# Optimization experiments

Hardware: AMD Instinct MI355X
Metric: run time of the kernel (lower is better)

The kernel has to match this reference:

```python
import jax, jax.numpy as jnp
import numpy as np

D = 128
N_DATA = 100000
N_TASK = 20000
E = 1000000


def _conv_params(key, d):
    ks = jax.random.split(key, 9)
    s = 1.0 / np.sqrt(d)
    return dict(
        Wmn=jax.random.uniform(ks[0], (d, d), jnp.float32, -s, s),
        bmn=jnp.zeros((d,), jnp.float32),
        Wme=jax.random.uniform(ks[1], (d, 1), jnp.float32, -1.0, 1.0),
        bme=jnp.zeros((d,), jnp.float32),
        Wgn=jax.random.uniform(ks[2], (d, d), jnp.float32, -s, s),
        bgn=jnp.zeros((d,), jnp.float32),
        Wge=jax.random.uniform(ks[3], (d, 1), jnp.float32, -1.0, 1.0),
        bge=jnp.zeros((d,), jnp.float32),
        bias=jnp.zeros((d,), jnp.float32),  # HeteConvLayer bias, zeros-init
    )


def setup_inputs() -> dict:
    key = jax.random.key(0)
    ks = jax.random.split(key, 12)
    inp = {
        'x_data': jax.random.normal(ks[0], (N_DATA, D), jnp.float32),
        'x_task': jax.random.normal(ks[1], (N_TASK, D), jnp.float32),
        'src_dt': jax.random.randint(ks[2], (E,), 0, N_DATA, jnp.int32),
        'dst_dt': jax.random.randint(ks[3], (E,), 0, N_TASK, jnp.int32),
        'ef_dt': jax.random.uniform(ks[4], (E, 1), jnp.float32),
        'src_td': jax.random.randint(ks[5], (E,), 0, N_TASK, jnp.int32),
        'dst_td': jax.random.randint(ks[6], (E,), 0, N_DATA, jnp.int32),
        'ef_td': jax.random.uniform(ks[7], (E, 1), jnp.float32),
    }
    # two separate HeteConvLayers (cfg.kg.hete=True)
    for name, k in (('dt', ks[8]), ('td', ks[9])):
        for pn, pv in _conv_params(k, D).items():
            inp[pn + '_' + name] = pv
    s = 1.0 / np.sqrt(D)
    inp['Ws_data'] = jax.random.uniform(ks[10], (D, D), jnp.float32, -s, s)
    inp['bs_data'] = jnp.zeros((D,), jnp.float32)
    inp['Ws_task'] = jax.random.uniform(ks[11], (D, D), jnp.float32, -s, s)
    inp['bs_task'] = jnp.zeros((D,), jnp.float32)
    return inp


def _hete_conv(x_neigh, src, dst, ef, Wmn, bmn, Wme, bme, Wgn, bgn, Wge, bge, bias, n_out):
    xj = x_neigh[src]                                   # [E, D] gather
    msg = xj @ Wmn.T + bmn + ef @ Wme.T + bme           # [E, D]
    gate = jax.nn.sigmoid(xj @ Wgn.T + bgn + ef @ Wge.T + bge) - 0.5  # gate_bias
    msg = msg * gate
    return jax.ops.segment_sum(msg, dst, num_segments=n_out) + bias


def _self_layer(x, Ws, bs):
    return (jax.nn.sigmoid(x @ Ws.T + bs) + 0.5) * x    # SelfLayer, gate_bias=True


def reference(x_data, x_task, src_dt, dst_dt, ef_dt, src_td, dst_td, ef_td,
              Wmn_dt, bmn_dt, Wme_dt, bme_dt, Wgn_dt, bgn_dt, Wge_dt, bge_dt, bias_dt,
              Wmn_td, bmn_td, Wme_td, bme_td, Wgn_td, bgn_td, Wge_td, bge_td, bias_td,
              Ws_data, bs_data, Ws_task, bs_task):
    # message type (data, property, task): neigh=data, self=task
    agg_task = _hete_conv(x_data, src_dt, dst_dt, ef_dt,
                          Wmn_dt, bmn_dt, Wme_dt, bme_dt,
                          Wgn_dt, bgn_dt, Wge_dt, bge_dt, bias_dt, N_TASK)
    # message type (task, property, data): neigh=task, self=data
    agg_data = _hete_conv(x_task, src_td, dst_td, ef_td,
                          Wmn_td, bmn_td, Wme_td, bme_td,
                          Wgn_td, bgn_td, Wge_td, bge_td, bias_td, N_DATA)
    # add self-transform, aggr='add', then Postlayer = ReLU
    data_emb = jax.nn.relu(agg_data + _self_layer(x_data, Ws_data, bs_data))
    task_emb = jax.nn.relu(agg_task + _self_layer(x_task, Ws_task, bs_task))
    # concatenate node-type outputs along node axis for a single output array
    return jnp.concatenate([data_emb, task_emb], axis=0)
```

## Files before the change

### kernel.cpp

```cpp
#include <hip/hip_runtime.h>
#include <hip/hip_bf16.h>
#include <cstdint>
#include <cstddef>

#define D_DIM 128

typedef __attribute__((ext_vector_type(8))) short short8;
typedef __attribute__((ext_vector_type(4))) float f32x4;

__device__ __forceinline__ float sigmoid_fast(float z) {
  return __builtin_amdgcn_rcpf(1.0f + __expf(-z));
}

__device__ __forceinline__ unsigned short f2bf(float f) {
  union { float f; unsigned u; } v; v.f = f;
  unsigned r = v.u + 0x7FFF + ((v.u >> 16) & 1);
  return (unsigned short)(r >> 16);
}
__device__ __forceinline__ float bf_lo(unsigned u) { return __uint_as_float(u << 16); }
__device__ __forceinline__ float bf_hi(unsigned u) { return __uint_as_float(u & 0xFFFF0000u); }

__global__ __launch_bounds__(256) void wconv_kernel(
    const float* __restrict__ s0, const float* __restrict__ s1, const float* __restrict__ s2,
    const float* __restrict__ s3, const float* __restrict__ s4, const float* __restrict__ s5,
    short* __restrict__ dst) {
  int idx = blockIdx.x * 256 + threadIdx.x;
  int mat = idx >> 12;
  int pos = (idx & 4095) * 4;
  const float* s = (mat == 0) ? s0 : (mat == 1) ? s1 : (mat == 2) ? s2
                 : (mat == 3) ? s3 : (mat == 4) ? s4 : s5;
  float4 f = *(const float4*)(s + pos);
  short4 o;
  o.x = (short)f2bf(f.x); o.y = (short)f2bf(f.y);
  o.z = (short)f2bf(f.z); o.w = (short)f2bf(f.w);
  *(short4*)(dst + mat * 16384 + pos) = o;
}

__global__ __launch_bounds__(256) void node_mfma_kernel(
    const float* __restrict__ x,
    const short* __restrict__ Wmnb, const short* __restrict__ Wgnb, const short* __restrict__ Wsb,
    const float* __restrict__ bmn, const float* __restrict__ bme,
    const float* __restrict__ bgn, const float* __restrict__ bge,
    const float* __restrict__ bs, const float* __restrict__ bias_other,
    unsigned int* __restrict__ YG, float* __restrict__ out_init, int n) {
  __shared__ unsigned sh[32][132];
  const int t = threadIdx.x;
  const int wave = t >> 6, lane = t & 63;
  const int q = lane >> 4, l15 = lane & 15;
  const int ng = wave >> 1;
  const int h = (wave & 1) * 64;
  const int base_node = blockIdx.x * 32;
  const int node_base = base_node + ng * 16;

  short8 a[4];
  {
    int m = node_base + l15;
    int mc = m < n ? m : (n - 1);
    const float* xrow = x + (size_t)mc * D_DIM;
#pragma unroll
    for (int ks = 0; ks < 4; ++ks) {
      float4 f0 = *(const float4*)(xrow + ks * 32 + q * 8);
      float4 f1 = *(const float4*)(xrow + ks * 32 + q * 8 + 4);
      union { short8 s; __hip_bfloat162 hh[4]; } u;
      u.hh[0] = __float22bfloat162_rn({f0.x, f0.y});
      u.hh[1] = __float22bfloat162_rn({f0.z, f0.w});
      u.hh[2] = __float22bfloat162_rn({f1.x, f1.y});
      u.hh[3] = __float22bfloat162_rn({f1.z, f1.w});
      a[ks] = u.s;
    }
  }

  f32x4 accY[4], accG[4], accS[4];
#pragma unroll
  for (int nt = 0; nt < 4; ++nt) { accY[nt] = {0,0,0,0}; accG[nt] = {0,0,0,0}; accS[nt] = {0,0,0,0}; }

#pragma unroll
  for (int nt = 0; nt < 4; ++nt) {
    const int row = h + nt * 16 + l15;
#pragma unroll
    for (int ks = 0; ks < 4; ++ks) {
      const int off = row * D_DIM + ks * 32 + q * 8;
      short8 bm  = *(const short8*)(Wmnb + off);
      short8 bg  = *(const short8*)(Wgnb + off);
      short8 bsw = *(const short8*)(Wsb + off);
      accY[nt] = __builtin_amdgcn_mfma_f32_16x16x32_bf16(a[ks], bm,  accY[nt], 0, 0, 0);
      accG[nt] = __builtin_amdgcn_mfma_f32_16x16x32_bf16(a[ks], bg,  accG[nt], 0, 0, 0);
      accS[nt] = __builtin_amdgcn_mfma_f32_16x16x32_bf16(a[ks], bsw, accS[nt], 0, 0, 0);
    }
  }

#pragma unroll
  for (int nt = 0; nt < 4; ++nt) {
    int d = h + nt * 16 + l15;
    float bmv = bmn[d] + bme[d];
    float bgv = bgn[d] + bge[d];
#pragma unroll
    for (int r = 0; r < 4; ++r) {
      union { __hip_bfloat162 hh; unsigned u; } pck;
      pck.hh = __float22bfloat162_rn({accY[nt][r] + bmv, accG[nt][r] + bgv});
      sh[ng * 16 + q * 4 + r][d] = pck.u;
    }
  }
  __syncthreads();
#pragma unroll
  for (int it = 0; it < 4; ++it) {
    int idx = (it * 256 + t) * 4;
    int nl = idx >> 7, dd = idx & 127;
    int node = base_node + nl;
    if (node < n)
      *(uint4*)(YG + (size_t)node * D_DIM + dd) = *(const uint4*)&sh[nl][dd];
  }
  __syncthreads();

  float* shf = (float*)sh;
#pragma unroll
  for (int nt = 0; nt < 4; ++nt) {
    int d = h + nt * 16 + l15;
    float bsv = bs[d];
#pragma unroll
    for (int r = 0; r < 4; ++r)
      shf[(ng * 16 + q * 4 + r) * 132 + d] = sigmoid_fast(accS[nt][r] + bsv) + 0.5f;
  }
  __syncthreads();
#pragma unroll
  for (int it = 0; it < 4; ++it) {
    int idx = (it * 256 + t) * 4;
    int nl = idx >> 7, dd = idx & 127;
    int node = base_node + nl;
    if (node < n) {
      float4 xv = *(const float4*)(x + (size_t)node * D_DIM + dd);
      float4 bo = *(const float4*)(bias_other + dd);
      const float* sp = &shf[nl * 132 + dd];
      float4 o;
      o.x = sp[0] * xv.x + bo.x;
      o.y = sp[1] * xv.y + bo.y;
      o.z = sp[2] * xv.z + bo.z;
      o.w = sp[3] * xv.w + bo.w;
      *(float4*)(out_init + (size_t)node * D_DIM + dd) = o;
    }
  }
}


__global__ __launch_bounds__(256) void hist0_kernel(
    const int* __restrict__ dst_dt, const int* __restrict__ dst_td,
    int* __restrict__ ghist, int nbt, int NB, int E) {
  __shared__ int lh[768];
  int t = threadIdx.x;
  lh[t] = 0; lh[t + 256] = 0; lh[t + 512] = 0;
  __syncthreads();
  for (int i = blockIdx.x * 256 + t; i < E; i += gridDim.x * 256) {
    atomicAdd(&lh[dst_dt[i] >> 6], 1);
    atomicAdd(&lh[nbt + (dst_td[i] >> 8)], 1);
  }
  __syncthreads();
#pragma unroll
  for (int k = 0; k < 3; ++k) {
    int b = t + k * 256;
    int c = lh[b];
    if (b < NB && c) atomicAdd(&ghist[b], c);
  }
}

__global__ __launch_bounds__(256) void bucket_scan_kernel(
    const int* __restrict__ ghist, int* __restrict__ bbase, int* __restrict__ bcur,
    int* __restrict__ offsets, int NB, int n_tot) {
  __shared__ int sc[256];
  int t = threadIdx.x;
  int i0 = t * 3;
  int c0 = (i0     < NB) ? ghist[i0]     : 0;
  int c1 = (i0 + 1 < NB) ? ghist[i0 + 1] : 0;
  int c2 = (i0 + 2 < NB) ? ghist[i0 + 2] : 0;
  int tot = c0 + c1 + c2;
  sc[t] = tot; __syncthreads();
  for (int s = 1; s < 256; s <<= 1) {
    int u = (t >= s) ? sc[t - s] : 0;
    __syncthreads(); sc[t] += u; __syncthreads();
  }
  int base = sc[t] - tot;
  if (i0     < NB) { bbase[i0]     = base;           bcur[i0]     = base; }
  if (i0 + 1 < NB) { bbase[i0 + 1] = base + c0;      bcur[i0 + 1] = base + c0; }
  if (i0 + 2 < NB) { bbase[i0 + 2] = base + c0 + c1; bcur[i0 + 2] = base + c0 + c1; }
  if (t == 255) { bbase[NB] = sc[255]; offsets[n_tot] = sc[255]; }
}

__global__ __launch_bounds__(256) void sort_a_kernel(
    const int* __restrict__ src_dt, const int* __restrict__ dst_dt, const float* __restrict__ ef_dt,
    const int* __restrict__ src_td, const int* __restrict__ dst_td, const float* __restrict__ ef_td,
    int* __restrict__ bcur, int2* __restrict__ eA, int nbt, int NB, int E) {
  __shared__ int lh[768];
  __shared__ int lcur[768];
  int t = threadIdx.x;
  lh[t] = 0; lh[t + 256] = 0; lh[t + 512] = 0;
  __syncthreads();
  int e0 = blockIdx.x * 4096;
  int e1 = min(E, e0 + 4096);
  for (int i = e0 + t; i < e1; i += 256) {
    atomicAdd(&lh[dst_dt[i] >> 6], 1);
    atomicAdd(&lh[nbt + (dst_td[i] >> 8)], 1);
  }
  __syncthreads();
#pragma unroll
  for (int k = 0; k < 3; ++k) {
    int b = t + k * 256;
    int c = lh[b];
    if (b < NB && c) lcur[b] = atomicAdd(&bcur[b], c);
  }
  __syncthreads();
  for (int i = e0 + t; i < e1; i += 256) {
    int c = dst_dt[i];
    int bkt = c >> 6;
    int pos = atomicAdd(&lcur[bkt], 1);
    eA[pos] = make_int2(src_dt[i],
        (int)((__float_as_uint(ef_dt[i]) & 0xFFFFFF00u) | (unsigned)(c & 63)));
    int cd = dst_td[i];
    int bkt2 = nbt + (cd >> 8);
    int pos2 = atomicAdd(&lcur[bkt2], 1);
    eA[pos2] = make_int2(src_td[i],
        (int)((__float_as_uint(ef_td[i]) & 0xFFFFFF00u) | (unsigned)(cd & 255)));
  }
}

__global__ __launch_bounds__(256) void sort_b_kernel(
    const int2* __restrict__ eA, const int* __restrict__ bbase,
    int* __restrict__ offsets, int2* __restrict__ eB,
    int nbt, int n_task, int n_tot) {
  __shared__ int lh[256], sc[256], lcur[256];
  int b = blockIdx.x, t = threadIdx.x;
  int base = bbase[b];
  int cnt = bbase[b + 1] - base;
  int c0, nloc;
  if (b < nbt) { c0 = b << 6; nloc = min(64, n_task - c0); }
  else { c0 = n_task + ((b - nbt) << 8); nloc = min(256, n_tot - c0); }
  lh[t] = 0; __syncthreads();
  for (int i = base + t; i < base + cnt; i += 256)
    atomicAdd(&lh[((unsigned)eA[i].y) & 255u], 1);
  __syncthreads();
  int v = lh[t];
  sc[t] = v; __syncthreads();
  for (int s = 1; s < 256; s <<= 1) {
    int u = (t >= s) ? sc[t - s] : 0;
    __syncthreads(); sc[t] += u; __syncthreads();
  }
  int ex = sc[t] - v;
  lcur[t] = base + ex;
  if (t < nloc) offsets[c0 + t] = base + ex;
  __syncthreads();
  for (int i = base + t; i < base + cnt; i += 256) {
    int2 e = eA[i];
    int pos = atomicAdd(&lcur[((unsigned)e.y) & 255u], 1);
    eB[pos] = e;
  }
}

__device__ __forceinline__ void gstep(float2& acc, int2 e, const unsigned* __restrict__ YG,
                                      int lane, float2 wme, float2 wge) {
  uint2 yg = *(const uint2*)(YG + (size_t)e.x * D_DIM + 2 * lane);
  float f = __int_as_float(e.y & (int)0xFFFFFF00);
  float g0 = sigmoid_fast(fmaf(f, wge.x, bf_hi(yg.x))) - 0.5f;
  float g1 = sigmoid_fast(fmaf(f, wge.y, bf_hi(yg.y))) - 0.5f;
  acc.x += fmaf(f, wme.x, bf_lo(yg.x)) * g0;
  acc.y += fmaf(f, wme.y, bf_lo(yg.y)) * g1;
}

__global__ __launch_bounds__(256) void gather_kernel(
    const unsigned* __restrict__ YG_dt, const unsigned* __restrict__ YG_td,
    const int* __restrict__ offsets, const int2* __restrict__ edata,
    const float* __restrict__ Wme_dt, const float* __restrict__ Wge_dt,
    const float* __restrict__ Wme_td, const float* __restrict__ Wge_td,
    float* __restrict__ out, int n_task, int n_data) {
  int w = (int)((blockIdx.x * 256u + threadIdx.x) >> 6);
  int lane = threadIdx.x & 63;
  if (w >= n_task + n_data) return;
  bool is_dt = w < n_task;
  const unsigned* YG = is_dt ? YG_dt : YG_td;
  const float* Wme = is_dt ? Wme_dt : Wme_td;
  const float* Wge = is_dt ? Wge_dt : Wge_td;
  size_t orow = is_dt ? (size_t)(n_data + w) : (size_t)(w - n_task);
  int beg = __builtin_amdgcn_readfirstlane(offsets[w]);
  int end = __builtin_amdgcn_readfirstlane(offsets[w + 1]);
  float2 wme = *(const float2*)(Wme + 2 * lane);
  float2 wge = *(const float2*)(Wge + 2 * lane);
  float* op = out + orow * D_DIM + 2 * lane;
  float2 acc = *(const float2*)op;
  int p = beg;
  for (; p + 4 <= end; p += 4) {
    int2 e0 = edata[p], e1 = edata[p + 1], e2 = edata[p + 2], e3 = edata[p + 3];
    gstep(acc, e0, YG, lane, wme, wge);
    gstep(acc, e1, YG, lane, wme, wge);
    gstep(acc, e2, YG, lane, wme, wge);
    gstep(acc, e3, YG, lane, wme, wge);
  }
  for (; p < end; ++p) gstep(acc, edata[p], YG, lane, wme, wge);
  acc.x = fmaxf(acc.x, 0.0f);
  acc.y = fmaxf(acc.y, 0.0f);
  *(float2*)op = acc;
}

extern "C" void kernel_launch(void* const* d_in, const int* in_sizes, int n_in,
                              void* d_out, int out_size, void* d_ws, size_t ws_size,
                              hipStream_t stream) {
  const float* x_data  = (const float*)d_in[0];
  const float* x_task  = (const float*)d_in[1];
  const int*   src_dt  = (const int*)d_in[2];
  const int*   dst_dt  = (const int*)d_in[3];
  const float* ef_dt   = (const float*)d_in[4];
  const int*   src_td  = (const int*)d_in[5];
  const int*   dst_td  = (const int*)d_in[6];
  const float* ef_td   = (const float*)d_in[7];
  const float* Wmn_dt  = (const float*)d_in[8];
  const float* bmn_dt  = (const float*)d_in[9];
  const float* Wme_dt  = (const float*)d_in[10];
  const float* bme_dt  = (const float*)d_in[11];
  const float* Wgn_dt  = (const float*)d_in[12];
  const float* bgn_dt  = (const float*)d_in[13];
  const float* Wge_dt  = (const float*)d_in[14];
  const float* bge_dt  = (const float*)d_in[15];
  const float* bias_dt = (const float*)d_in[16];
  const float* Wmn_td  = (const float*)d_in[17];
  const float* bmn_td  = (const float*)d_in[18];
  const float* Wme_td  = (const float*)d_in[19];
  const float* bme_td  = (const float*)d_in[20];
  const float* Wgn_td  = (const float*)d_in[21];
  const float* bgn_td  = (const float*)d_in[22];
  const float* Wge_td  = (const float*)d_in[23];
  const float* bge_td  = (const float*)d_in[24];
  const float* bias_td = (const float*)d_in[25];
  const float* Ws_data = (const float*)d_in[26];
  const float* bs_data = (const float*)d_in[27];
  const float* Ws_task = (const float*)d_in[28];
  const float* bs_task = (const float*)d_in[29];
  float* out = (float*)d_out;

  const int N_DATA = in_sizes[0] / D_DIM;
  const int N_TASK = in_sizes[1] / D_DIM;
  const int E = in_sizes[2];
  const int N_TOT = N_TASK + N_DATA;
  const int NBT = (N_TASK + 63) >> 6;
  const int NBD = (N_DATA + 255) >> 8;
  const int NB = NBT + NBD;

  char* ws = (char*)d_ws;
  size_t off = 0;
  auto alloc = [&](size_t bytes) { void* p = ws + off; off += (bytes + 255) & ~(size_t)255; return p; };
  unsigned int* YG_dt = (unsigned int*)alloc((size_t)N_DATA * D_DIM * 4);
  unsigned int* YG_td = (unsigned int*)alloc((size_t)N_TASK * D_DIM * 4);
  int2* eA     = (int2*)alloc((size_t)2 * E * 8);
  int2* eB     = (int2*)alloc((size_t)2 * E * 8);
  int*  offs   = (int*)alloc((size_t)(N_TOT + 1) * 4);
  int*  ghist  = (int*)alloc(768 * 4);
  int*  bbase  = (int*)alloc(768 * 4);
  int*  bcur   = (int*)alloc(768 * 4);
  short* Wb    = (short*)alloc((size_t)6 * 16384 * 2);
  (void)ws_size; (void)n_in; (void)out_size;

  hipMemsetAsync(ghist, 0, 768 * 4, stream);

  wconv_kernel<<<96, 256, 0, stream>>>(Wmn_dt, Wgn_dt, Ws_data, Wmn_td, Wgn_td, Ws_task, Wb);

  node_mfma_kernel<<<(N_DATA + 31) / 32, 256, 0, stream>>>(
      x_data, Wb, Wb + 16384, Wb + 32768,
      bmn_dt, bme_dt, bgn_dt, bge_dt, bs_data, bias_td,
      YG_dt, out, N_DATA);
  node_mfma_kernel<<<(N_TASK + 31) / 32, 256, 0, stream>>>(
      x_task, Wb + 3 * 16384, Wb + 4 * 16384, Wb + 5 * 16384,
      bmn_td, bme_td, bgn_td, bge_td, bs_task, bias_dt,
      YG_td, out + (size_t)N_DATA * D_DIM, N_TASK);

  hist0_kernel<<<256, 256, 0, stream>>>(dst_dt, dst_td, ghist, NBT, NB, E);
  bucket_scan_kernel<<<1, 256, 0, stream>>>(ghist, bbase, bcur, offs, NB, N_TOT);
  sort_a_kernel<<<(E + 4095) / 4096, 256, 0, stream>>>(
      src_dt, dst_dt, ef_dt, src_td, dst_td, ef_td, bcur, eA, NBT, NB, E);
  sort_b_kernel<<<NB, 256, 0, stream>>>(eA, bbase, offs, eB, NBT, N_TASK, N_TOT);

  gather_kernel<<<(N_TOT + 3) / 4, 256, 0, stream>>>(
      YG_dt, YG_td, offs, eB, Wme_dt, Wge_dt, Wme_td, Wge_td, out, N_TASK, N_DATA);
}
```

Baseline: 496.0 us.

## Replace second sort pass with per-bucket shared-memory atomic gather

Drops the fine-grained sort_b pass and the per-node offsets. Data-side buckets now use 64 nodes each, like task buckets, so there are up to 2048 buckets. Each gather block owns one bucket, accumulates messages into a 64x128 float LDS tile using shared-memory atomics, then adds the tile to the output and applies ReLU. This removes one full read/write pass over the 2E edge records, but adds LDS atomic contention, a 32KB LDS footprint per block that limits occupancy, and non-deterministic summation order.

```diff
diff --git a/kernel.cpp b/kernel.cpp
--- a/kernel.cpp
+++ b/kernel.cpp
@@ -145,17 +145,18 @@
 __global__ __launch_bounds__(256) void hist0_kernel(
     const int* __restrict__ dst_dt, const int* __restrict__ dst_td,
     int* __restrict__ ghist, int nbt, int NB, int E) {
-  __shared__ int lh[768];
+  __shared__ int lh[2048];
   int t = threadIdx.x;
-  lh[t] = 0; lh[t + 256] = 0; lh[t + 512] = 0;
+#pragma unroll
+  for (int k = 0; k < 8; ++k) lh[t + k * 256] = 0;
   __syncthreads();
   for (int i = blockIdx.x * 256 + t; i < E; i += gridDim.x * 256) {
     atomicAdd(&lh[dst_dt[i] >> 6], 1);
-    atomicAdd(&lh[nbt + (dst_td[i] >> 8)], 1);
-  }
-  __syncthreads();
-#pragma unroll
-  for (int k = 0; k < 3; ++k) {
+    atomicAdd(&lh[nbt + (dst_td[i] >> 6)], 1);
+  }
+  __syncthreads();
+#pragma unroll
+  for (int k = 0; k < 8; ++k) {
     int b = t + k * 256;
     int c = lh[b];
     if (b < NB && c) atomicAdd(&ghist[b], c);
@@ -163,45 +164,46 @@
 }
 
 __global__ __launch_bounds__(256) void bucket_scan_kernel(
-    const int* __restrict__ ghist, int* __restrict__ bbase, int* __restrict__ bcur,
-    int* __restrict__ offsets, int NB, int n_tot) {
+    const int* __restrict__ ghist, int* __restrict__ bbase, int* __restrict__ bcur, int NB) {
   __shared__ int sc[256];
   int t = threadIdx.x;
-  int i0 = t * 3;
-  int c0 = (i0     < NB) ? ghist[i0]     : 0;
-  int c1 = (i0 + 1 < NB) ? ghist[i0 + 1] : 0;
-  int c2 = (i0 + 2 < NB) ? ghist[i0 + 2] : 0;
-  int tot = c0 + c1 + c2;
+  int i0 = t * 8;
+  int c[8]; int tot = 0;
+#pragma unroll
+  for (int k = 0; k < 8; ++k) { c[k] = (i0 + k < NB) ? ghist[i0 + k] : 0; tot += c[k]; }
   sc[t] = tot; __syncthreads();
   for (int s = 1; s < 256; s <<= 1) {
     int u = (t >= s) ? sc[t - s] : 0;
     __syncthreads(); sc[t] += u; __syncthreads();
   }
-  int base = sc[t] - tot;
-  if (i0     < NB) { bbase[i0]     = base;           bcur[i0]     = base; }
-  if (i0 + 1 < NB) { bbase[i0 + 1] = base + c0;      bcur[i0 + 1] = base + c0; }
-  if (i0 + 2 < NB) { bbase[i0 + 2] = base + c0 + c1; bcur[i0 + 2] = base + c0 + c1; }
-  if (t == 255) { bbase[NB] = sc[255]; offsets[n_tot] = sc[255]; }
+  int run = sc[t] - tot;
+#pragma unroll
+  for (int k = 0; k < 8; ++k) {
+    if (i0 + k < NB) { bbase[i0 + k] = run; bcur[i0 + k] = run; }
+    run += c[k];
+  }
+  if (t == 255) bbase[NB] = run;
 }
 
 __global__ __launch_bounds__(256) void sort_a_kernel(
     const int* __restrict__ src_dt, const int* __restrict__ dst_dt, const float* __restrict__ ef_dt,
     const int* __restrict__ src_td, const int* __restrict__ dst_td, const float* __restrict__ ef_td,
     int* __restrict__ bcur, int2* __restrict__ eA, int nbt, int NB, int E) {
-  __shared__ int lh[768];
-  __shared__ int lcur[768];
+  __shared__ int lh[2048];
+  __shared__ int lcur[2048];
   int t = threadIdx.x;
-  lh[t] = 0; lh[t + 256] = 0; lh[t + 512] = 0;
+#pragma unroll
+  for (int k = 0; k < 8; ++k) lh[t + k * 256] = 0;
   __syncthreads();
   int e0 = blockIdx.x * 4096;
   int e1 = min(E, e0 + 4096);
   for (int i = e0 + t; i < e1; i += 256) {
     atomicAdd(&lh[dst_dt[i] >> 6], 1);
-    atomicAdd(&lh[nbt + (dst_td[i] >> 8)], 1);
-  }
-  __syncthreads();
-#pragma unroll
-  for (int k = 0; k < 3; ++k) {
+    atomicAdd(&lh[nbt + (dst_td[i] >> 6)], 1);
+  }
+  __syncthreads();
+#pragma unroll
+  for (int k = 0; k < 8; ++k) {
     int b = t + k * 256;
     int c = lh[b];
     if (b < NB && c) lcur[b] = atomicAdd(&bcur[b], c);
@@ -209,92 +211,93 @@
   __syncthreads();
   for (int i = e0 + t; i < e1; i += 256) {
     int c = dst_dt[i];
-    int bkt = c >> 6;
-    int pos = atomicAdd(&lcur[bkt], 1);
+    int pos = atomicAdd(&lcur[c >> 6], 1);
     eA[pos] = make_int2(src_dt[i],
         (int)((__float_as_uint(ef_dt[i]) & 0xFFFFFF00u) | (unsigned)(c & 63)));
     int cd = dst_td[i];
-    int bkt2 = nbt + (cd >> 8);
-    int pos2 = atomicAdd(&lcur[bkt2], 1);
+    int pos2 = atomicAdd(&lcur[nbt + (cd >> 6)], 1);
     eA[pos2] = make_int2(src_td[i],
-        (int)((__float_as_uint(ef_td[i]) & 0xFFFFFF00u) | (unsigned)(cd & 255)));
-  }
-}
-
-__global__ __launch_bounds__(256) void sort_b_kernel(
-    const int2* __restrict__ eA, const int* __restrict__ bbase,
-    int* __restrict__ offsets, int2* __restrict__ eB,
-    int nbt, int n_task, int n_tot) {
-  __shared__ int lh[256], sc[256], lcur[256];
-  int b = blockIdx.x, t = threadIdx.x;
-  int base = bbase[b];
-  int cnt = bbase[b + 1] - base;
-  int c0, nloc;
-  if (b < nbt) { c0 = b << 6; nloc = min(64, n_task - c0); }
-  else { c0 = n_task + ((b - nbt) << 8); nloc = min(256, n_tot - c0); }
-  lh[t] = 0; __syncthreads();
-  for (int i = base + t; i < base + cnt; i += 256)
-    atomicAdd(&lh[((unsigned)eA[i].y) & 255u], 1);
-  __syncthreads();
-  int v = lh[t];
-  sc[t] = v; __syncthreads();
-  for (int s = 1; s < 256; s <<= 1) {
-    int u = (t >= s) ? sc[t - s] : 0;
-    __syncthreads(); sc[t] += u; __syncthreads();
-  }
-  int ex = sc[t] - v;
-  lcur[t] = base + ex;
-  if (t < nloc) offsets[c0 + t] = base + ex;
-  __syncthreads();
-  for (int i = base + t; i < base + cnt; i += 256) {
-    int2 e = eA[i];
-    int pos = atomicAdd(&lcur[((unsigned)e.y) & 255u], 1);
-    eB[pos] = e;
-  }
-}
-
-__device__ __forceinline__ void gstep(float2& acc, int2 e, const unsigned* __restrict__ YG,
-                                      int lane, float2 wme, float2 wge) {
-  uint2 yg = *(const uint2*)(YG + (size_t)e.x * D_DIM + 2 * lane);
-  float f = __int_as_float(e.y & (int)0xFFFFFF00);
-  float g0 = sigmoid_fast(fmaf(f, wge.x, bf_hi(yg.x))) - 0.5f;
-  float g1 = sigmoid_fast(fmaf(f, wge.y, bf_hi(yg.y))) - 0.5f;
-  acc.x += fmaf(f, wme.x, bf_lo(yg.x)) * g0;
-  acc.y += fmaf(f, wme.y, bf_lo(yg.y)) * g1;
-}
-
-__global__ __launch_bounds__(256) void gather_kernel(
+        (int)((__float_as_uint(ef_td[i]) & 0xFFFFFF00u) | (unsigned)(cd & 63)));
+  }
+}
+
+__global__ __launch_bounds__(256) void gather_bucket_kernel(
     const unsigned* __restrict__ YG_dt, const unsigned* __restrict__ YG_td,
-    const int* __restrict__ offsets, const int2* __restrict__ edata,
+    const int* __restrict__ bbase, const int2* __restrict__ eA,
     const float* __restrict__ Wme_dt, const float* __restrict__ Wge_dt,
     const float* __restrict__ Wme_td, const float* __restrict__ Wge_td,
-    float* __restrict__ out, int n_task, int n_data) {
-  int w = (int)((blockIdx.x * 256u + threadIdx.x) >> 6);
-  int lane = threadIdx.x & 63;
-  if (w >= n_task + n_data) return;
-  bool is_dt = w < n_task;
+    float* __restrict__ out, int nbt, int n_task, int n_data) {
+  __shared__ float accum[64 * 128];
+  const int b = blockIdx.x, t = threadIdx.x;
+  const int wave = t >> 6, lane = t & 63;
+  const bool is_dt = b < nbt;
   const unsigned* YG = is_dt ? YG_dt : YG_td;
   const float* Wme = is_dt ? Wme_dt : Wme_td;
   const float* Wge = is_dt ? Wge_dt : Wge_td;
-  size_t orow = is_dt ? (size_t)(n_data + w) : (size_t)(w - n_task);
-  int beg = __builtin_amdgcn_readfirstlane(offsets[w]);
-  int end = __builtin_amdgcn_readfirstlane(offsets[w + 1]);
-  float2 wme = *(const float2*)(Wme + 2 * lane);
-  float2 wge = *(const float2*)(Wge + 2 * lane);
-  float* op = out + orow * D_DIM + 2 * lane;
-  float2 acc = *(const float2*)op;
-  int p = beg;
-  for (; p + 4 <= end; p += 4) {
-    int2 e0 = edata[p], e1 = edata[p + 1], e2 = edata[p + 2], e3 = edata[p + 3];
-    gstep(acc, e0, YG, lane, wme, wge);
-    gstep(acc, e1, YG, lane, wme, wge);
-    gstep(acc, e2, YG, lane, wme, wge);
-    gstep(acc, e3, YG, lane, wme, wge);
-  }
-  for (; p < end; ++p) gstep(acc, edata[p], YG, lane, wme, wge);
-  acc.x = fmaxf(acc.x, 0.0f);
-  acc.y = fmaxf(acc.y, 0.0f);
-  *(float2*)op = acc;
+  const int d0 = is_dt ? (b << 6) : ((b - nbt) << 6);
+  const int row0 = is_dt ? (n_data + d0) : d0;
+  const int nloc = is_dt ? min(64, n_task - d0) : min(64, n_data - d0);
+
+#pragma unroll
+  for (int k = 0; k < 8; ++k)
+    *(float4*)&accum[(k * 256 + t) * 4] = {0.f, 0.f, 0.f, 0.f};
+
+  const float wme0 = Wme[lane], wme1 = Wme[lane + 64];
+  const float wge0 = Wge[lane], wge1 = Wge[lane + 64];
+  __syncthreads();
+
+  const int base = bbase[b], end = bbase[b + 1];
+  int p = base + wave;
+  for (; p + 4 < end; p += 8) {
+    int2 ea = eA[p], eb = eA[p + 4];
+    size_t ra = (size_t)ea.x << 7, rb = (size_t)eb.x << 7;
+    unsigned a0 = YG[ra + lane], a1 = YG[ra + lane + 64];
+    unsigned b0 = YG[rb + lane], b1 = YG[rb + lane + 64];
+    float fa = __int_as_float(ea.y & (int)0xFFFFFF00);
+    float fb = __int_as_float(eb.y & (int)0xFFFFFF00);
+    int la = ea.y & 63, lb = eb.y & 63;
+    float ga0 = sigmoid_fast(fmaf(fa, wge0, bf_hi(a0))) - 0.5f;
+    float ga1 = sigmoid_fast(fmaf(fa, wge1, bf_hi(a1))) - 0.5f;
+    float ma0 = fmaf(fa, wme0, bf_lo(a0)) * ga0;
+    float ma1 = fmaf(fa, wme1, bf_lo(a1)) * ga1;
+    atomicAdd(&accum[la * 128 + lane], ma0);
+    atomicAdd(&accum[la * 128 + lane + 64], ma1);
+    float gb0 = sigmoid_fast(fmaf(fb, wge0, bf_hi(b0))) - 0.5f;
+    float gb1 = sigmoid_fast(fmaf(fb, wge1, bf_hi(b1))) - 0.5f;
+    float mb0 = fmaf(fb, wme0, bf_lo(b0)) * gb0;
+    float mb1 = fmaf(fb, wme1, bf_lo(b1)) * gb1;
+    atomicAdd(&accum[lb * 128 + lane], mb0);
+    atomicAdd(&accum[lb * 128 + lane + 64], mb1);
+  }
+  for (; p < end; p += 4) {
+    int2 ea = eA[p];
+    size_t ra = (size_t)ea.x << 7;
+    unsigned a0 = YG[ra + lane], a1 = YG[ra + lane + 64];
+    float fa = __int_as_float(ea.y & (int)0xFFFFFF00);
+    int la = ea.y & 63;
+    float ga0 = sigmoid_fast(fmaf(fa, wge0, bf_hi(a0))) - 0.5f;
+    float ga1 = sigmoid_fast(fmaf(fa, wge1, bf_hi(a1))) - 0.5f;
+    atomicAdd(&accum[la * 128 + lane], fmaf(fa, wme0, bf_lo(a0)) * ga0);
+    atomicAdd(&accum[la * 128 + lane + 64], fmaf(fa, wme1, bf_lo(a1)) * ga1);
+  }
+  __syncthreads();
+
+#pragma unroll
+  for (int k = 0; k < 8; ++k) {
+    int idx = (k * 256 + t) * 4;
+    int loc = idx >> 7, dd = idx & 127;
+    if (loc < nloc) {
+      float* op = out + (size_t)(row0 + loc) * D_DIM + dd;
+      float4 ov = *(const float4*)op;
+      float4 av = *(const float4*)&accum[loc * 128 + dd];
+      float4 r;
+      r.x = fmaxf(ov.x + av.x, 0.f);
+      r.y = fmaxf(ov.y + av.y, 0.f);
+      r.z = fmaxf(ov.z + av.z, 0.f);
+      r.w = fmaxf(ov.w + av.w, 0.f);
+      *(float4*)op = r;
+    }
+  }
 }
 
 extern "C" void kernel_launch(void* const* d_in, const int* in_sizes, int n_in,
@@ -335,9 +338,8 @@
   const int N_DATA = in_sizes[0] / D_DIM;
   const int N_TASK = in_sizes[1] / D_DIM;
   const int E = in_sizes[2];
-  const int N_TOT = N_TASK + N_DATA;
   const int NBT = (N_TASK + 63) >> 6;
-  const int NBD = (N_DATA + 255) >> 8;
+  const int NBD = (N_DATA + 63) >> 6;
   const int NB = NBT + NBD;
 
   char* ws = (char*)d_ws;
@@ -346,15 +348,13 @@
   unsigned int* YG_dt = (unsigned int*)alloc((size_t)N_DATA * D_DIM * 4);
   unsigned int* YG_td = (unsigned int*)alloc((size_t)N_TASK * D_DIM * 4);
   int2* eA     = (int2*)alloc((size_t)2 * E * 8);
-  int2* eB     = (int2*)alloc((size_t)2 * E * 8);
-  int*  offs   = (int*)alloc((size_t)(N_TOT + 1) * 4);
-  int*  ghist  = (int*)alloc(768 * 4);
-  int*  bbase  = (int*)alloc(768 * 4);
-  int*  bcur   = (int*)alloc(768 * 4);
+  int*  ghist  = (int*)alloc(2048 * 4);
+  int*  bbase  = (int*)alloc(2064 * 4);
+  int*  bcur   = (int*)alloc(2048 * 4);
   short* Wb    = (short*)alloc((size_t)6 * 16384 * 2);
   (void)ws_size; (void)n_in; (void)out_size;
 
-  hipMemsetAsync(ghist, 0, 768 * 4, stream);
+  hipMemsetAsync(ghist, 0, 2048 * 4, stream);
 
   wconv_kernel<<<96, 256, 0, stream>>>(Wmn_dt, Wgn_dt, Ws_data, Wmn_td, Wgn_td, Ws_task, Wb);
 
@@ -368,11 +368,11 @@
       YG_td, out + (size_t)N_DATA * D_DIM, N_TASK);
 
   hist0_kernel<<<256, 256, 0, stream>>>(dst_dt, dst_td, ghist, NBT, NB, E);
-  bucket_scan_kernel<<<1, 256, 0, stream>>>(ghist, bbase, bcur, offs, NB, N_TOT);
+  bucket_scan_kernel<<<1, 256, 0, stream>>>(ghist, bbase, bcur, NB);
   sort_a_kernel<<<(E + 4095) / 4096, 256, 0, stream>>>(
       src_dt, dst_dt, ef_dt, src_td, dst_td, ef_td, bcur, eA, NBT, NB, E);
-  sort_b_kernel<<<NB, 256, 0, stream>>>(eA, bbase, offs, eB, NBT, N_TASK, N_TOT);
-
-  gather_kernel<<<(N_TOT + 3) / 4, 256, 0, stream>>>(
-      YG_dt, YG_td, offs, eB, Wme_dt, Wge_dt, Wme_td, Wge_td, out, N_TASK, N_DATA);
-}
+
+  gather_bucket_kernel<<<NB, 256, 0, stream>>>(
+      YG_dt, YG_td, bbase, eA, Wme_dt, Wge_dt, Wme_td, Wge_td,
+      out, NBT, N_TASK, N_DATA);
+}
```

After: 1.741 ms. +251.0%, slower.
